# Optimization experiments

Measured on AMD Instinct MI355X. Metric: run time of the kernel, lower is better.

Reference implementation:

```python
import jax, jax.numpy as jnp
import numpy as np

N_ATOMS, N_BONDS, MAX_NB = 100000, 200000, 6
HIDDEN, DEPTH = 256, 6
ATOM_FDIM, BOND_FDIM = 39, 11


def setup_inputs() -> dict:
    key = jax.random.key(0)
    ks = jax.random.split(key, 6)
    fatoms = jax.random.normal(ks[0], (N_ATOMS, ATOM_FDIM), dtype=jnp.float32)
    fbonds = jax.random.normal(ks[1], (N_BONDS, BOND_FDIM), dtype=jnp.float32)
    # indices into message rows [0, N_BONDS); row 0 is the zero-padding row
    aoutgraph = jax.random.randint(ks[2], (N_ATOMS, MAX_NB), 0, N_BONDS)
    # (x, y) atom-index pairs; entry 0 is padding (unused)
    all_bonds = jax.random.randint(ks[3], (N_BONDS, 2), 0, N_ATOMS)
    # learned params (Linear layers, bias=False): y = x @ W.T
    W_nin = jax.random.normal(ks[4], (HIDDEN, ATOM_FDIM), dtype=jnp.float32) * 0.1
    W_node = jax.random.normal(ks[5], (HIDDEN, HIDDEN + BOND_FDIM), dtype=jnp.float32) * 0.05
    return {"fatoms": fatoms, "fbonds": fbonds, "aoutgraph": aoutgraph,
            "all_bonds": all_bonds, "W_nin": W_nin, "W_node": W_node}


def reference(fatoms, fbonds, aoutgraph, all_bonds, W_nin, W_node):
    # h0 = relu(W_nin @ fatoms); original keeps H_n as [hidden, n_atoms],
    # we keep [n_atoms, hidden] and transpose only at the end (same math).
    h0 = jax.nn.relu(fatoms @ W_nin.T)              # [N, H]
    in_n = all_bonds[1:, 1]                          # target atom of bonds 1..B-1
    zero_row = jnp.zeros((1, HIDDEN), dtype=h0.dtype)
    Hn = h0
    for _ in range(DEPTH):
        # message b = H_n[:, y_b] for b>=1, zero row at b=0, concat bond feats
        atom_msg = jnp.concatenate([zero_row, Hn[in_n]], axis=0)   # [B, H]
        message = jnp.concatenate([atom_msg, fbonds], axis=1)      # [B, H+11]
        # gather neighbor bond messages per atom and sum-aggregate
        nei = message[aoutgraph].sum(axis=1)                       # [N, H+11]
        Hn = jax.nn.relu(h0 + nei @ W_node.T)                      # [N, H]
    return Hn.T                                                    # [H, N] as original
```

## Files before the change

### kernel.cpp

```cpp
#include <hip/hip_runtime.h>

#define N_ATOMS 100000
#define N_BONDS 200000
#define MAX_NB 6
#define HIDDEN 256
#define DEPTH 6
#define ATOM_FDIM 39
#define BOND_FDIM 11
#define WNODE_COLS (HIDDEN + BOND_FDIM)

typedef __attribute__((ext_vector_type(8))) short bf16x8;
typedef __attribute__((ext_vector_type(4))) short s16x4;
typedef __attribute__((ext_vector_type(4))) float f32x4;

__device__ __forceinline__ unsigned short f2bf(float x) {
  unsigned u = __float_as_uint(x);
  unsigned r = (u + 0x7FFFu + ((u >> 16) & 1u)) >> 16;
  return (unsigned short)r;
}
__device__ __forceinline__ float bf2f(unsigned short h) {
  return __uint_as_float(((unsigned)h) << 16);
}
__device__ __forceinline__ void split3(float x, short* s1, short* s2, short* s3) {
  unsigned short h1 = f2bf(x);
  float r1 = x - bf2f(h1);
  unsigned short h2 = f2bf(r1);
  float r2 = r1 - bf2f(h2);
  *s1 = (short)h1;
  *s2 = (short)h2;
  *s3 = (short)f2bf(r2);
}

union U4 { short s[4]; s16x4 v; };

__global__ __launch_bounds__(256) void split_w_kernel(
    const float* __restrict__ W, short* __restrict__ Bsp) {
  int g = blockIdx.x * 256 + threadIdx.x;
  int n = g >> 6;
  int k4 = (g & 63) * 4;
  const float* wp = &W[(size_t)n * WNODE_COLS + k4];
  int o = n * 256 + k4;
#pragma unroll
  for (int j = 0; j < 4; ++j) {
    short a, b, c;
    split3(wp[j], &a, &b, &c);
    Bsp[o + j] = a;
    Bsp[65536 + o + j] = b;
    Bsp[131072 + o + j] = c;
  }
}

__global__ __launch_bounds__(256) void init_kernel(
    const float* __restrict__ fatoms,
    const float* __restrict__ fbonds,
    const int* __restrict__ aoutgraph,
    const float* __restrict__ W_nin,
    const float* __restrict__ W_node,
    float* __restrict__ Hn,
    float* __restrict__ base) {
  __shared__ float Wn_lds[ATOM_FDIM * 256];
  __shared__ float Wf_lds[BOND_FDIM * 256];
  __shared__ float fa_lds[32 * 40];
  __shared__ float fs_lds[32 * 12];
  int tid = threadIdx.x;
  int a0 = blockIdx.x * 32;

  for (int k = 0; k < ATOM_FDIM; ++k)
    Wn_lds[k * 256 + tid] = W_nin[tid * ATOM_FDIM + k];
  for (int k = 0; k < BOND_FDIM; ++k)
    Wf_lds[k * 256 + tid] = W_node[tid * WNODE_COLS + HIDDEN + k];
  {
    int a_l = tid >> 3, j8 = tid & 7;
#pragma unroll
    for (int jj = 0; jj < 5; ++jj) {
      int k = j8 * 5 + jj;
      if (k < ATOM_FDIM)
        fa_lds[a_l * 40 + k] = fatoms[(size_t)(a0 + a_l) * ATOM_FDIM + k];
    }
  }
  for (int i = tid; i < 384; i += 256) {
    int a_l = i / 12, f = i - a_l * 12;
    if (f < BOND_FDIM) {
      float s = 0.f;
#pragma unroll
      for (int nb = 0; nb < MAX_NB; ++nb) {
        int b = aoutgraph[(size_t)(a0 + a_l) * MAX_NB + nb];
        s += fbonds[(size_t)b * BOND_FDIM + f];
      }
      fs_lds[a_l * 12 + f] = s;
    }
  }
  __syncthreads();

  int l = tid & 63, w = tid >> 6;
  f32x4 acc1[8] = {};
  f32x4 acc2[8] = {};
  for (int k = 0; k < ATOM_FDIM; ++k) {
    f32x4 wv = *(const f32x4*)&Wn_lds[k * 256 + l * 4];
#pragma unroll
    for (int ai = 0; ai < 8; ++ai) {
      float av = fa_lds[(w * 8 + ai) * 40 + k];
      acc1[ai] += wv * av;
    }
  }
  for (int k = 0; k < BOND_FDIM; ++k) {
    f32x4 wv = *(const f32x4*)&Wf_lds[k * 256 + l * 4];
#pragma unroll
    for (int ai = 0; ai < 8; ++ai) {
      float av = fs_lds[(w * 8 + ai) * 12 + k];
      acc2[ai] += wv * av;
    }
  }
#pragma unroll
  for (int ai = 0; ai < 8; ++ai) {
    int a_g = a0 + w * 8 + ai;
    size_t off = (size_t)a_g * HIDDEN + l * 4;
    f32x4 h0v, bs;
#pragma unroll
    for (int j = 0; j < 4; ++j) {
      float h0j = fmaxf(acc1[ai][j], 0.f);
      h0v[j] = h0j;
      bs[j] = h0j + acc2[ai][j];
    }
    *(f32x4*)&Hn[off] = h0v;
    *(f32x4*)&base[off] = bs;
  }
}

#define KCH 32
#define AST 40

__global__ __launch_bounds__(256, 3) void fused_kernel(
    const float* __restrict__ Hn_in,
    const float* __restrict__ base,
    const short* __restrict__ Bsp,
    const int* __restrict__ aout,
    const int* __restrict__ bonds,
    float* __restrict__ Hn_out) {
  __shared__ short As[2][3][32 * AST];
  __shared__ int src_lds[192];
  int tid = threadIdx.x;
  int a0 = blockIdx.x * 32;

  if (tid < 192) {
    int a_l = tid / 6, nb = tid - a_l * 6;
    int b = aout[(size_t)(a0 + a_l) * MAX_NB + nb];
    src_lds[tid] = (b != 0) ? bonds[2 * b + 1] : -1;
  }
  __syncthreads();

  int lane = tid & 63, w = tid >> 6;
  int lr = lane & 15, lk = lane >> 4;
  int r_a = tid >> 3, q = tid & 7;

  const char* hb = (const char*)Hn_in;
  unsigned voff[MAX_NB];
  float gw[MAX_NB];
#pragma unroll
  for (int nb = 0; nb < MAX_NB; ++nb) {
    int s = src_lds[r_a * 6 + nb];
    int sr = s >= 0 ? s : 0;
    gw[nb] = s >= 0 ? 1.f : 0.f;
    voff[nb] = (unsigned)((sr * HIDDEN + q * 4) * 4);
  }
  int ao_st = r_a * AST + q * 4;

  f32x4 acc[2][4] = {};

  {
    f32x4 v = {0.f, 0.f, 0.f, 0.f};
#pragma unroll
    for (int nb = 0; nb < MAX_NB; ++nb)
      v += *(const f32x4*)(hb + voff[nb]) * gw[nb];
    U4 t1, t2, t3;
#pragma unroll
    for (int j = 0; j < 4; ++j) split3(v[j], &t1.s[j], &t2.s[j], &t3.s[j]);
    *(s16x4*)&As[0][0][ao_st] = t1.v;
    *(s16x4*)&As[0][1][ao_st] = t2.v;
    *(s16x4*)&As[0][2][ao_st] = t3.v;
  }
  __syncthreads();

#pragma unroll
  for (int c = 0; c < 8; ++c) {
    const int cur = c & 1;
    bf16x8 b0[4], b1[4], b2[4];
#pragma unroll
    for (int n = 0; n < 4; ++n) {
      int bo = (w * 64 + n * 16 + lr) * 256 + c * KCH + lk * 8;
      b0[n] = *(const bf16x8*)&Bsp[bo];
      b1[n] = *(const bf16x8*)&Bsp[65536 + bo];
      b2[n] = *(const bf16x8*)&Bsp[131072 + bo];
    }
    f32x4 ga[MAX_NB];
    if (c < 7) {
#pragma unroll
      for (int nb = 0; nb < MAX_NB; ++nb)
        ga[nb] = *(const f32x4*)(hb + voff[nb] + (c + 1) * KCH * 4);
    }
    __builtin_amdgcn_sched_barrier(0);
    __builtin_amdgcn_s_setprio(1);
#pragma unroll
    for (int m = 0; m < 2; ++m) {
      int ao = (m * 16 + lr) * AST + lk * 8;
      bf16x8 af0 = *(const bf16x8*)&As[cur][0][ao];
      bf16x8 af1 = *(const bf16x8*)&As[cur][1][ao];
      bf16x8 af2 = *(const bf16x8*)&As[cur][2][ao];
#pragma unroll
      for (int n = 0; n < 4; ++n) {
        f32x4 cc = acc[m][n];
        cc = __builtin_amdgcn_mfma_f32_16x16x32_bf16(af0, b0[n], cc, 0, 0, 0);
        cc = __builtin_amdgcn_mfma_f32_16x16x32_bf16(af0, b1[n], cc, 0, 0, 0);
        cc = __builtin_amdgcn_mfma_f32_16x16x32_bf16(af1, b0[n], cc, 0, 0, 0);
        cc = __builtin_amdgcn_mfma_f32_16x16x32_bf16(af1, b1[n], cc, 0, 0, 0);
        cc = __builtin_amdgcn_mfma_f32_16x16x32_bf16(af0, b2[n], cc, 0, 0, 0);
        cc = __builtin_amdgcn_mfma_f32_16x16x32_bf16(af2, b0[n], cc, 0, 0, 0);
        acc[m][n] = cc;
      }
    }
    __builtin_amdgcn_s_setprio(0);
    if (c < 7) {
      f32x4 v = {0.f, 0.f, 0.f, 0.f};
#pragma unroll
      for (int nb = 0; nb < MAX_NB; ++nb) v += ga[nb] * gw[nb];
      U4 t1, t2, t3;
#pragma unroll
      for (int j = 0; j < 4; ++j) split3(v[j], &t1.s[j], &t2.s[j], &t3.s[j]);
      *(s16x4*)&As[cur ^ 1][0][ao_st] = t1.v;
      *(s16x4*)&As[cur ^ 1][1][ao_st] = t2.v;
      *(s16x4*)&As[cur ^ 1][2][ao_st] = t3.v;
      __syncthreads();
    }
  }

#pragma unroll
  for (int m = 0; m < 2; ++m) {
    int row0 = a0 + m * 16 + lk * 4;
#pragma unroll
    for (int n = 0; n < 4; ++n) {
      int col = w * 64 + n * 16 + lr;
#pragma unroll
      for (int r = 0; r < 4; ++r) {
        size_t off = (size_t)(row0 + r) * HIDDEN + col;
        float b = __builtin_nontemporal_load(&base[off]);
        float v = fmaxf(b + acc[m][n][r], 0.f);
        __builtin_nontemporal_store(v, &Hn_out[off]);
      }
    }
  }
}

__global__ __launch_bounds__(256) void transpose_kernel(
    const float* __restrict__ Hn, float* __restrict__ out) {
  __shared__ float tile[64][68];
  int a0 = blockIdx.x * 64, h0 = blockIdx.y * 64;
  int tid = threadIdx.x;
#pragma unroll
  for (int p = 0; p < 2; ++p) {
    int id = tid + p * 256;
    int r = id >> 3, c8 = (id & 7) * 8;
    int ag = a0 + r;
    if (ag > N_ATOMS - 1) ag = N_ATOMS - 1;
    const float* hp = &Hn[(size_t)ag * HIDDEN + h0 + c8];
    *(f32x4*)&tile[r][c8] = *(const f32x4*)hp;
    *(f32x4*)&tile[r][c8 + 4] = *(const f32x4*)(hp + 4);
  }
  __syncthreads();
  int h = tid >> 2, as = (tid & 3) * 16;
  size_t ob = (size_t)(h0 + h) * N_ATOMS + a0 + as;
  if (a0 + 64 <= N_ATOMS) {
#pragma unroll
    for (int q = 0; q < 4; ++q) {
      f32x4 v;
#pragma unroll
      for (int j = 0; j < 4; ++j) v[j] = tile[as + q * 4 + j][h];
      __builtin_nontemporal_store(v, (f32x4*)&out[ob + q * 4]);
    }
  } else {
    for (int j = 0; j < 16; ++j)
      if (a0 + as + j < N_ATOMS)
        __builtin_nontemporal_store(tile[as + j][h], &out[ob + j]);
  }
}

extern "C" void kernel_launch(void* const* d_in, const int* in_sizes, int n_in,
                              void* d_out, int out_size, void* d_ws, size_t ws_size,
                              hipStream_t stream) {
  const float* fatoms = (const float*)d_in[0];
  const float* fbonds = (const float*)d_in[1];
  const int* aoutgraph = (const int*)d_in[2];
  const int* all_bonds = (const int*)d_in[3];
  const float* W_nin = (const float*)d_in[4];
  const float* W_node = (const float*)d_in[5];
  float* out = (float*)d_out;

  const size_t NH = (size_t)N_ATOMS * HIDDEN;
  float* base = (float*)d_ws;
  float* HnA = base + NH;
  short* Bsp = (short*)(HnA + NH);
  float* HnB = out;

  split_w_kernel<<<64, 256, 0, stream>>>(W_node, Bsp);
  init_kernel<<<N_ATOMS / 32, 256, 0, stream>>>(fatoms, fbonds, aoutgraph,
                                                W_nin, W_node, HnA, base);

  const int nblk = N_ATOMS / 32;
  for (int it = 0; it < DEPTH; ++it) {
    const float* in = (it & 1) ? HnB : HnA;
    float* o = (it & 1) ? HnA : HnB;
    fused_kernel<<<nblk, 256, 0, stream>>>(in, base, Bsp, aoutgraph,
                                           all_bonds, o);
  }
  dim3 tgrid((N_ATOMS + 63) / 64, HIDDEN / 64);
  transpose_kernel<<<tgrid, 256, 0, stream>>>(HnA, out);
}
```

Baseline: 1.478 ms.

## Gather neighbor sums directly into MFMA A-fragments, dropping LDS staging

The fused message-passing kernel now builds each wave's A operand in registers. Each lane gathers and sums its own 8 hidden values per neighbor, then splits them into three bf16 parts, so the shared-memory A buffer and per-chunk barriers are gone. Blocks shrink from 32 to 16 atoms, so each atom's neighbor sum is computed redundantly by all 4 waves. The grid doubles, and occupancy hints drop to 2 blocks per CU because more registers are live. This trades LDS traffic and syncs for 4x redundant gathers, each hitting L2, and more weight-fragment loads per atom.

```diff
diff --git a/kernel.cpp b/kernel.cpp
--- a/kernel.cpp
+++ b/kernel.cpp
@@ -10,7 +10,6 @@
 #define WNODE_COLS (HIDDEN + BOND_FDIM)
 
 typedef __attribute__((ext_vector_type(8))) short bf16x8;
-typedef __attribute__((ext_vector_type(4))) short s16x4;
 typedef __attribute__((ext_vector_type(4))) float f32x4;
 
 __device__ __forceinline__ unsigned short f2bf(float x) {
@@ -31,7 +30,7 @@
   *s3 = (short)f2bf(r2);
 }
 
-union U4 { short s[4]; s16x4 v; };
+union U8 { short s[8]; bf16x8 v; };
 
 __global__ __launch_bounds__(256) void split_w_kernel(
     const float* __restrict__ W, short* __restrict__ Bsp) {
@@ -127,125 +126,105 @@
   }
 }
 
-#define KCH 32
-#define AST 40
-
-__global__ __launch_bounds__(256, 3) void fused_kernel(
+__global__ __launch_bounds__(256, 2) void fused_kernel(
     const float* __restrict__ Hn_in,
     const float* __restrict__ base,
     const short* __restrict__ Bsp,
     const int* __restrict__ aout,
     const int* __restrict__ bonds,
     float* __restrict__ Hn_out) {
-  __shared__ short As[2][3][32 * AST];
-  __shared__ int src_lds[192];
   int tid = threadIdx.x;
-  int a0 = blockIdx.x * 32;
-
-  if (tid < 192) {
-    int a_l = tid / 6, nb = tid - a_l * 6;
-    int b = aout[(size_t)(a0 + a_l) * MAX_NB + nb];
-    src_lds[tid] = (b != 0) ? bonds[2 * b + 1] : -1;
-  }
-  __syncthreads();
-
   int lane = tid & 63, w = tid >> 6;
   int lr = lane & 15, lk = lane >> 4;
-  int r_a = tid >> 3, q = tid & 7;
-
-  const char* hb = (const char*)Hn_in;
+  int a0 = blockIdx.x * 16;
+  int arow = a0 + lr;
+
   unsigned voff[MAX_NB];
   float gw[MAX_NB];
 #pragma unroll
   for (int nb = 0; nb < MAX_NB; ++nb) {
-    int s = src_lds[r_a * 6 + nb];
-    int sr = s >= 0 ? s : 0;
-    gw[nb] = s >= 0 ? 1.f : 0.f;
-    voff[nb] = (unsigned)((sr * HIDDEN + q * 4) * 4);
-  }
-  int ao_st = r_a * AST + q * 4;
-
-  f32x4 acc[2][4] = {};
-
-  {
-    f32x4 v = {0.f, 0.f, 0.f, 0.f};
-#pragma unroll
-    for (int nb = 0; nb < MAX_NB; ++nb)
-      v += *(const f32x4*)(hb + voff[nb]) * gw[nb];
-    U4 t1, t2, t3;
-#pragma unroll
-    for (int j = 0; j < 4; ++j) split3(v[j], &t1.s[j], &t2.s[j], &t3.s[j]);
-    *(s16x4*)&As[0][0][ao_st] = t1.v;
-    *(s16x4*)&As[0][1][ao_st] = t2.v;
-    *(s16x4*)&As[0][2][ao_st] = t3.v;
-  }
-  __syncthreads();
+    int b = aout[(size_t)arow * MAX_NB + nb];
+    int s = (b != 0) ? bonds[2 * b + 1] : 0;
+    gw[nb] = (b != 0) ? 1.f : 0.f;
+    voff[nb] = (unsigned)((s * HIDDEN + lk * 8) * 4);
+  }
+  const char* hb = (const char*)Hn_in;
+
+  const short* bp0 = Bsp + (w * 64 + lr) * 256 + lk * 8;
+  const short* bp1 = bp0 + 65536;
+  const short* bp2 = bp0 + 131072;
+
+  f32x4 acc[4] = {};
+
+  f32x4 gA[MAX_NB], gB[MAX_NB];
+#pragma unroll
+  for (int nb = 0; nb < MAX_NB; ++nb) {
+    gA[nb] = *(const f32x4*)(hb + voff[nb]);
+    gB[nb] = *(const f32x4*)(hb + voff[nb] + 16);
+  }
 
 #pragma unroll
   for (int c = 0; c < 8; ++c) {
-    const int cur = c & 1;
     bf16x8 b0[4], b1[4], b2[4];
 #pragma unroll
     for (int n = 0; n < 4; ++n) {
-      int bo = (w * 64 + n * 16 + lr) * 256 + c * KCH + lk * 8;
-      b0[n] = *(const bf16x8*)&Bsp[bo];
-      b1[n] = *(const bf16x8*)&Bsp[65536 + bo];
-      b2[n] = *(const bf16x8*)&Bsp[131072 + bo];
-    }
-    f32x4 ga[MAX_NB];
+      int bo = n * 4096 + c * 32;
+      b0[n] = *(const bf16x8*)(bp0 + bo);
+      b1[n] = *(const bf16x8*)(bp1 + bo);
+      b2[n] = *(const bf16x8*)(bp2 + bo);
+    }
+    __builtin_amdgcn_sched_barrier(0);
+    f32x4 nA[MAX_NB], nB[MAX_NB];
     if (c < 7) {
 #pragma unroll
-      for (int nb = 0; nb < MAX_NB; ++nb)
-        ga[nb] = *(const f32x4*)(hb + voff[nb] + (c + 1) * KCH * 4);
+      for (int nb = 0; nb < MAX_NB; ++nb) {
+        nA[nb] = *(const f32x4*)(hb + voff[nb] + (c + 1) * 128);
+        nB[nb] = *(const f32x4*)(hb + voff[nb] + (c + 1) * 128 + 16);
+      }
     }
     __builtin_amdgcn_sched_barrier(0);
+    f32x4 vlo = {0.f, 0.f, 0.f, 0.f}, vhi = {0.f, 0.f, 0.f, 0.f};
+#pragma unroll
+    for (int nb = 0; nb < MAX_NB; ++nb) {
+      vlo += gA[nb] * gw[nb];
+      vhi += gB[nb] * gw[nb];
+    }
+    U8 t1, t2, t3;
+#pragma unroll
+    for (int j = 0; j < 4; ++j) split3(vlo[j], &t1.s[j], &t2.s[j], &t3.s[j]);
+#pragma unroll
+    for (int j = 0; j < 4; ++j)
+      split3(vhi[j], &t1.s[4 + j], &t2.s[4 + j], &t3.s[4 + j]);
     __builtin_amdgcn_s_setprio(1);
 #pragma unroll
-    for (int m = 0; m < 2; ++m) {
-      int ao = (m * 16 + lr) * AST + lk * 8;
-      bf16x8 af0 = *(const bf16x8*)&As[cur][0][ao];
-      bf16x8 af1 = *(const bf16x8*)&As[cur][1][ao];
-      bf16x8 af2 = *(const bf16x8*)&As[cur][2][ao];
-#pragma unroll
-      for (int n = 0; n < 4; ++n) {
-        f32x4 cc = acc[m][n];
-        cc = __builtin_amdgcn_mfma_f32_16x16x32_bf16(af0, b0[n], cc, 0, 0, 0);
-        cc = __builtin_amdgcn_mfma_f32_16x16x32_bf16(af0, b1[n], cc, 0, 0, 0);
-        cc = __builtin_amdgcn_mfma_f32_16x16x32_bf16(af1, b0[n], cc, 0, 0, 0);
-        cc = __builtin_amdgcn_mfma_f32_16x16x32_bf16(af1, b1[n], cc, 0, 0, 0);
-        cc = __builtin_amdgcn_mfma_f32_16x16x32_bf16(af0, b2[n], cc, 0, 0, 0);
-        cc = __builtin_amdgcn_mfma_f32_16x16x32_bf16(af2, b0[n], cc, 0, 0, 0);
-        acc[m][n] = cc;
-      }
+    for (int n = 0; n < 4; ++n) {
+      f32x4 cc = acc[n];
+      cc = __builtin_amdgcn_mfma_f32_16x16x32_bf16(t1.v, b0[n], cc, 0, 0, 0);
+      cc = __builtin_amdgcn_mfma_f32_16x16x32_bf16(t1.v, b1[n], cc, 0, 0, 0);
+      cc = __builtin_amdgcn_mfma_f32_16x16x32_bf16(t2.v, b0[n], cc, 0, 0, 0);
+      cc = __builtin_amdgcn_mfma_f32_16x16x32_bf16(t2.v, b1[n], cc, 0, 0, 0);
+      cc = __builtin_amdgcn_mfma_f32_16x16x32_bf16(t1.v, b2[n], cc, 0, 0, 0);
+      cc = __builtin_amdgcn_mfma_f32_16x16x32_bf16(t3.v, b0[n], cc, 0, 0, 0);
+      acc[n] = cc;
     }
     __builtin_amdgcn_s_setprio(0);
     if (c < 7) {
-      f32x4 v = {0.f, 0.f, 0.f, 0.f};
-#pragma unroll
-      for (int nb = 0; nb < MAX_NB; ++nb) v += ga[nb] * gw[nb];
-      U4 t1, t2, t3;
-#pragma unroll
-      for (int j = 0; j < 4; ++j) split3(v[j], &t1.s[j], &t2.s[j], &t3.s[j]);
-      *(s16x4*)&As[cur ^ 1][0][ao_st] = t1.v;
-      *(s16x4*)&As[cur ^ 1][1][ao_st] = t2.v;
-      *(s16x4*)&As[cur ^ 1][2][ao_st] = t3.v;
-      __syncthreads();
-    }
-  }
-
-#pragma unroll
-  for (int m = 0; m < 2; ++m) {
-    int row0 = a0 + m * 16 + lk * 4;
+#pragma unroll
+      for (int nb = 0; nb < MAX_NB; ++nb) {
+        gA[nb] = nA[nb];
+        gB[nb] = nB[nb];
+      }
+    }
+  }
+
+  size_t ebase = (size_t)(a0 + lk * 4) * HIDDEN + w * 64 + lr;
+#pragma unroll
+  for (int r = 0; r < 4; ++r) {
 #pragma unroll
     for (int n = 0; n < 4; ++n) {
-      int col = w * 64 + n * 16 + lr;
-#pragma unroll
-      for (int r = 0; r < 4; ++r) {
-        size_t off = (size_t)(row0 + r) * HIDDEN + col;
-        float b = __builtin_nontemporal_load(&base[off]);
-        float v = fmaxf(b + acc[m][n][r], 0.f);
-        __builtin_nontemporal_store(v, &Hn_out[off]);
-      }
+      size_t off = ebase + (size_t)r * HIDDEN + n * 16;
+      float b = __builtin_nontemporal_load(&base[off]);
+      __builtin_nontemporal_store(fmaxf(b + acc[n][r], 0.f), &Hn_out[off]);
     }
   }
 }
@@ -304,7 +283,7 @@
   init_kernel<<<N_ATOMS / 32, 256, 0, stream>>>(fatoms, fbonds, aoutgraph,
                                                 W_nin, W_node, HnA, base);
 
-  const int nblk = N_ATOMS / 32;
+  const int nblk = N_ATOMS / 16;
   for (int it = 0; it < DEPTH; ++it) {
     const float* in = (it & 1) ? HnB : HnA;
     float* o = (it & 1) ? HnA : HnB;
```

New measurement: 3.732 ms. 2.53x slower.
